# Performance work log

Hardware: AMD Instinct MI355X
Metric: run time of the kernel (lower is better)

The kernel has to match this reference:

```python
import jax, jax.numpy as jnp
import numpy as np

N_HEAD = 16
HEAD_DIM = 64
EPS = 1e-5
ROPE_BASE = 10000.0


def setup_inputs() -> dict:
    key = jax.random.key(0)
    ks = jax.random.split(key, 3)
    B, T, C = 4, 2048, 1024
    x = jax.random.normal(ks[0], (B, T, C), dtype=jnp.float32)
    Wqkv = jax.random.normal(ks[1], (C, 3 * C), dtype=jnp.float32) * (C ** -0.5)
    Wproj = jax.random.normal(ks[2], (C, C), dtype=jnp.float32) * (C ** -0.5)
    q_norm_w = jnp.ones((HEAD_DIM,), dtype=jnp.float32)
    k_norm_w = jnp.ones((HEAD_DIM,), dtype=jnp.float32)
    return {"x": x, "Wqkv": Wqkv, "Wproj": Wproj, "q_norm_w": q_norm_w, "k_norm_w": k_norm_w}


def _rms_norm(x, w):
    xf = x.astype(jnp.float32)
    normed = xf * jax.lax.rsqrt(jnp.mean(xf * xf, axis=-1, keepdims=True) + EPS)
    return (normed * w).astype(x.dtype)


def _rope_tables(T, dtype):
    inv_freq = 1.0 / (ROPE_BASE ** (jnp.arange(0, HEAD_DIM, 2, dtype=jnp.float32) / HEAD_DIM))
    t = jnp.arange(T, dtype=jnp.float32)
    freqs = jnp.outer(t, inv_freq)              # [T, D/2]
    emb = jnp.concatenate([freqs, freqs], -1)   # [T, D]
    return jnp.cos(emb).astype(dtype), jnp.sin(emb).astype(dtype)


def _rotate_half(x):
    x1, x2 = jnp.split(x, 2, axis=-1)
    return jnp.concatenate([-x2, x1], axis=-1)


def reference(x, Wqkv, Wproj, q_norm_w, k_norm_w):
    B, T, C = x.shape
    qkv = x @ Wqkv                               # [B, T, 3C]
    q, k, v = jnp.split(qkv, 3, axis=-1)
    # [B, H, T, D]
    q = q.reshape(B, T, N_HEAD, HEAD_DIM).transpose(0, 2, 1, 3)
    k = k.reshape(B, T, N_HEAD, HEAD_DIM).transpose(0, 2, 1, 3)
    v = v.reshape(B, T, N_HEAD, HEAD_DIM).transpose(0, 2, 1, 3)
    # per-head QK RMSNorm
    q = _rms_norm(q, q_norm_w)
    k = _rms_norm(k, k_norm_w)
    # RoPE
    cos, sin = _rope_tables(T, q.dtype)          # [T, D] broadcast over B,H
    q = q * cos + _rotate_half(q) * sin
    k = k * cos + _rotate_half(k) * sin
    # causal attention
    scale = 1.0 / np.sqrt(HEAD_DIM)
    att = jnp.einsum('bhqd,bhkd->bhqk', q, k) * scale
    causal = jnp.tril(jnp.ones((T, T), dtype=bool))
    att = jnp.where(causal, att, -jnp.inf)
    att = jax.nn.softmax(att, axis=-1)
    y = jnp.einsum('bhqk,bhkd->bhqd', att, v)    # [B, H, T, D]
    y = y.transpose(0, 2, 1, 3).reshape(B, T, C)
    return y @ Wproj
```

## Files before the change

kernel.cpp:

```cpp
#include <hip/hip_runtime.h>
#include <cstdint>
#include <type_traits>

typedef __attribute__((ext_vector_type(8))) short bf16x8;
typedef __attribute__((ext_vector_type(4))) float f32x4;

typedef unsigned int __attribute__((address_space(1))) as1_uint;
typedef unsigned int __attribute__((address_space(3))) as3_uint;

__device__ __forceinline__ void llds16(const void* g, void* l) {
  __builtin_amdgcn_global_load_lds((const as1_uint*)g, (as3_uint*)l, 16, 0, 0);
}

__device__ __forceinline__ unsigned short f2bf(float f) {
  unsigned int u = __builtin_bit_cast(unsigned int, f);
  u = (u + 0x7fffu + ((u >> 16) & 1u)) >> 16;
  return (unsigned short)u;
}
__device__ __forceinline__ float bf2f(unsigned short h) {
  unsigned int u = ((unsigned int)h) << 16;
  return __builtin_bit_cast(float, u);
}

__global__ __launch_bounds__(256) void cvt_f32_bf16(const float* __restrict__ in,
                                                    unsigned short* __restrict__ out, int n4) {
  int i = blockIdx.x * blockDim.x + threadIdx.x;
  int stride = gridDim.x * blockDim.x;
  for (; i < n4; i += stride) {
    float4 v = ((const float4*)in)[i];
    uint2 p;
    p.x = (unsigned)f2bf(v.x) | ((unsigned)f2bf(v.y) << 16);
    p.y = (unsigned)f2bf(v.z) | ((unsigned)f2bf(v.w) << 16);
    ((uint2*)out)[i] = p;
  }
}

__global__ __launch_bounds__(256) void transpose_f32_bf16(const float* __restrict__ W,
                                                          unsigned short* __restrict__ Wt,
                                                          int K, int N) {
  __shared__ float tile[64][65];
  int n0 = blockIdx.x * 64, k0 = blockIdx.y * 64;
  int t = threadIdx.x;
  int lr = t >> 4, lc = (t & 15) * 4;
#pragma unroll
  for (int i = 0; i < 4; ++i) {
    int k = lr + i * 16;
    float4 v = *(const float4*)&W[(size_t)(k0 + k) * N + n0 + lc];
    tile[k][lc] = v.x; tile[k][lc + 1] = v.y; tile[k][lc + 2] = v.z; tile[k][lc + 3] = v.w;
  }
  __syncthreads();
  int n = t >> 2, kc = (t & 3) * 16;
  unsigned short* dst = &Wt[(size_t)(n0 + n) * K + k0 + kc];
#pragma unroll
  for (int j = 0; j < 16; ++j) dst[j] = f2bf(tile[kc + j][n]);
}

__global__ __launch_bounds__(256) void rope_tabT(float* __restrict__ cosT, float* __restrict__ sinT) {
  int i = blockIdx.x * 256 + threadIdx.x;
  int dm = i >> 11, t = i & 2047;
  float inv = powf(10000.0f, -(float)dm * (1.0f / 32.0f));
  float a = (float)t * inv;
  cosT[i] = cosf(a);
  sinT[i] = sinf(a);
}

__device__ __forceinline__ void block_map(int& bx, int& by) {
  const int lin = blockIdx.y * gridDim.x + blockIdx.x;
  const int xcd = lin & 7;
  const int idx = lin >> 3;
  const int ych = gridDim.y >> 3;
  by = xcd * ych + (idx & (ych - 1));
  bx = idx / ych;
}

template <typename OutT>
__global__ __launch_bounds__(256) void gemm_ring(const unsigned short* __restrict__ A,
                                                 const unsigned short* __restrict__ Bt,
                                                 OutT* __restrict__ C, int M, int N, int K) {
  __shared__ unsigned short As[3][128 * 32];
  __shared__ unsigned short Bs[3][128 * 32];
  const int tid = threadIdx.x;
  const int w = tid >> 6, lane = tid & 63;
  const int l15 = lane & 15, lg = lane >> 4;
  const int wr = w >> 1, wc = w & 1;

  int bx, by;
  block_map(bx, by);
  const int m0 = by * 128, n0 = bx * 128;

  const size_t K2 = (size_t)K * 2;
  const char* Ag = (const char*)A;
  const char* Bg = (const char*)Bt;
  const int rc = lane >> 2;
  const int cb = (lane & 3) * 16;

  auto stage = [&](int buf, int kt) {
#pragma unroll
    for (int i = 0; i < 2; ++i) {
      int c = w + i * 4;
      int row = c * 16 + rc;
      int srcc = cb ^ (((row >> 1) & 3) << 4);
      size_t kofs = (size_t)kt * 64 + srcc;
      llds16(Ag + (size_t)(m0 + row) * K2 + kofs, (char*)&As[buf][0] + c * 1024);
      llds16(Bg + (size_t)(n0 + row) * K2 + kofs, (char*)&Bs[buf][0] + c * 1024);
    }
  };

  f32x4 acc[4][4] = {};
  const int nk = K >> 5;
  stage(0, 0);
  stage(1, 1);
  int cur = 0;
  for (int t = 0; t < nk; ++t) {
    if (t + 1 < nk) asm volatile("s_waitcnt vmcnt(4)" ::: "memory");
    else            asm volatile("s_waitcnt vmcnt(0)" ::: "memory");
    __builtin_amdgcn_s_barrier();
    asm volatile("" ::: "memory");
    if (t + 2 < nk) stage(cur + 2 >= 3 ? cur - 1 : cur + 2, t + 2);

    const unsigned short* Ab = &As[cur][0];
    const unsigned short* Bb = &Bs[cur][0];
    bf16x8 af[4], bfr[4];
#pragma unroll
    for (int m = 0; m < 4; ++m) {
      int row = wr * 64 + m * 16 + l15;
      af[m] = *(const bf16x8*)((const char*)Ab + row * 64 + ((lg * 16) ^ (((row >> 1) & 3) << 4)));
    }
#pragma unroll
    for (int n = 0; n < 4; ++n) {
      int row = wc * 64 + n * 16 + l15;
      bfr[n] = *(const bf16x8*)((const char*)Bb + row * 64 + ((lg * 16) ^ (((row >> 1) & 3) << 4)));
    }
#pragma unroll
    for (int m = 0; m < 4; ++m)
#pragma unroll
      for (int n = 0; n < 4; ++n)
        acc[m][n] = __builtin_amdgcn_mfma_f32_16x16x32_bf16(af[m], bfr[n], acc[m][n], 0, 0, 0);
    cur = (cur == 2) ? 0 : cur + 1;
  }

#pragma unroll
  for (int m = 0; m < 4; ++m)
#pragma unroll
    for (int n = 0; n < 4; ++n) {
      int row = m0 + wr * 64 + m * 16 + lg * 4;
      int col = n0 + wc * 64 + n * 16 + l15;
#pragma unroll
      for (int r = 0; r < 4; ++r) {
        if constexpr (std::is_same<OutT, float>::value)
          C[(size_t)(row + r) * N + col] = acc[m][n][r];
        else
          C[(size_t)(row + r) * N + col] = f2bf(acc[m][n][r]);
      }
    }
}

__global__ __launch_bounds__(256) void gemm_qkv(const unsigned short* __restrict__ A,
                                                const unsigned short* __restrict__ Bt,
                                                const float* __restrict__ qw,
                                                const float* __restrict__ kw,
                                                const float* __restrict__ cosTT,
                                                const float* __restrict__ sinTT,
                                                unsigned short* __restrict__ Qr,
                                                unsigned short* __restrict__ Kr,
                                                unsigned short* __restrict__ Vtg) {
  constexpr int K = 1024;
  __shared__ unsigned short smem[6 * 128 * 32];
  unsigned short* As = smem;
  unsigned short* Bs = smem + 3 * 128 * 32;

  const int tid = threadIdx.x;
  const int w = tid >> 6, lane = tid & 63;
  const int l15 = lane & 15, lg = lane >> 4;
  const int wr = w >> 1, wc = w & 1;

  int bx, by;
  block_map(bx, by);
  const int m0 = by * 128, n0 = bx * 128;

  const size_t K2 = (size_t)K * 2;
  const char* Ag = (const char*)A;
  const char* Bg = (const char*)Bt;
  const int rc = lane >> 2;
  const int cb = (lane & 3) * 16;

  auto stage = [&](int buf, int kt) {
#pragma unroll
    for (int i = 0; i < 2; ++i) {
      int c = w + i * 4;
      int row = c * 16 + rc;
      int srcc = cb ^ (((row >> 1) & 3) << 4);
      size_t kofs = (size_t)kt * 64 + srcc;
      llds16(Ag + (size_t)(m0 + row) * K2 + kofs, (char*)As + buf * 8192 + c * 1024);
      llds16(Bg + (size_t)(n0 + row) * K2 + kofs, (char*)Bs + buf * 8192 + c * 1024);
    }
  };

  f32x4 acc[4][4] = {};
  const int nk = K >> 5;
  stage(0, 0);
  stage(1, 1);
  int cur = 0;
  for (int t = 0; t < nk; ++t) {
    if (t + 1 < nk) asm volatile("s_waitcnt vmcnt(4)" ::: "memory");
    else            asm volatile("s_waitcnt vmcnt(0)" ::: "memory");
    __builtin_amdgcn_s_barrier();
    asm volatile("" ::: "memory");
    if (t + 2 < nk) stage(cur + 2 >= 3 ? cur - 1 : cur + 2, t + 2);

    const char* Ab = (const char*)As + cur * 8192;
    const char* Bb = (const char*)Bs + cur * 8192;
    bf16x8 af[4], bfr[4];
#pragma unroll
    for (int m = 0; m < 4; ++m) {
      int row = wr * 64 + m * 16 + l15;
      af[m] = *(const bf16x8*)(Ab + row * 64 + ((lg * 16) ^ (((row >> 1) & 3) << 4)));
    }
#pragma unroll
    for (int n = 0; n < 4; ++n) {
      int row = wc * 64 + n * 16 + l15;
      bfr[n] = *(const bf16x8*)(Bb + row * 64 + ((lg * 16) ^ (((row >> 1) & 3) << 4)));
    }
#pragma unroll
    for (int m = 0; m < 4; ++m)
#pragma unroll
      for (int n = 0; n < 4; ++n)
        acc[m][n] = __builtin_amdgcn_mfma_f32_16x16x32_bf16(af[m], bfr[n], acc[m][n], 0, 0, 0);
    cur = (cur == 2) ? 0 : cur + 1;
  }

  __syncthreads();
  const int cls = bx >> 3;
  const int head = (bx & 7) * 2 + wc;
  const int rowb = m0 + wr * 64;
  const int b = rowb >> 11;
  const int tl = rowb & 2047;
  const int bh = b * 16 + head;
  unsigned short* tb = smem + w * (64 * 76);

  if (cls < 2) {
    const float* wt = cls ? kw : qw;
    const float scale = cls ? 1.0f : 0.18033688011112042f;
    unsigned short* outp = cls ? Kr : Qr;
    float wv[4];
#pragma unroll
    for (int n = 0; n < 4; ++n) wv[n] = wt[n * 16 + l15];
    const float* c0p = cosTT + l15 * 2048;
    const float* c1p = cosTT + (16 + l15) * 2048;
    const float* s0p = sinTT + l15 * 2048;
    const float* s1p = sinTT + (16 + l15) * 2048;
#pragma unroll
    for (int m = 0; m < 4; ++m) {
      int t0 = tl + m * 16 + lg * 4;
      f32x4 ssq = {};
#pragma unroll
      for (int n = 0; n < 4; ++n) ssq += acc[m][n] * acc[m][n];
#pragma unroll
      for (int r = 0; r < 4; ++r) {
        float v = ssq[r];
        v += __shfl_xor(v, 1); v += __shfl_xor(v, 2);
        v += __shfl_xor(v, 4); v += __shfl_xor(v, 8);
        ssq[r] = rsqrtf(v * (1.0f / 64.0f) + 1e-5f) * scale;
      }
      f32x4 nv[4];
#pragma unroll
      for (int n = 0; n < 4; ++n) nv[n] = acc[m][n] * ssq * wv[n];
      f32x4 cv0 = *(const f32x4*)(c0p + t0);
      f32x4 cv1 = *(const f32x4*)(c1p + t0);
      f32x4 sv0 = *(const f32x4*)(s0p + t0);
      f32x4 sv1 = *(const f32x4*)(s1p + t0);
      f32x4 ov[4];
      ov[0] = nv[0] * cv0 - nv[2] * sv0;
      ov[1] = nv[1] * cv1 - nv[3] * sv1;
      ov[2] = nv[2] * cv0 + nv[0] * sv0;
      ov[3] = nv[3] * cv1 + nv[1] * sv1;
      int tloc = m * 16 + lg * 4;
#pragma unroll
      for (int n = 0; n < 4; ++n)
#pragma unroll
        for (int r = 0; r < 4; ++r)
          tb[(tloc + r) * 76 + n * 16 + l15] = f2bf(ov[n][r]);
    }
    asm volatile("" ::: "memory");
    const int t = lane;
    unsigned short* yp = outp + ((size_t)bh * 2048 + tl + t) * 64;
#pragma unroll
    for (int j = 0; j < 8; ++j)
      *(bf16x8*)(yp + j * 8) = *(const bf16x8*)(tb + t * 76 + j * 8);
  } else {
#pragma unroll
    for (int m = 0; m < 4; ++m)
#pragma unroll
      for (int n = 0; n < 4; ++n) {
        int d = n * 16 + l15, t = m * 16 + lg * 4;
        ushort4 pk;
        pk.x = f2bf(acc[m][n][0]); pk.y = f2bf(acc[m][n][1]);
        pk.z = f2bf(acc[m][n][2]); pk.w = f2bf(acc[m][n][3]);
        *(ushort4*)(tb + d * 76 + t) = pk;
      }
    asm volatile("" ::: "memory");
    int d2 = lane;
    unsigned short* vp = Vtg + ((size_t)bh * 64 + d2) * 2048 + tl;
#pragma unroll
    for (int j = 0; j < 8; ++j) {
      bf16x8 vv = *(const bf16x8*)(tb + d2 * 76 + j * 8);
      *(bf16x8*)(vp + j * 8) = vv;
    }
  }
}

__global__ __launch_bounds__(256) void attn_fwd(const unsigned short* __restrict__ Q,
                                                const unsigned short* __restrict__ K,
                                                const unsigned short* __restrict__ Vtg,
                                                unsigned short* __restrict__ Y) {
  const int bh = blockIdx.x;
  const int pr = blockIdx.y;
  const int b = bh >> 4, h = bh & 15;
  const int tid = threadIdx.x;
  const int w = tid >> 6, lane = tid & 63;
  const int l15 = lane & 15, lg = lane >> 4;

  __shared__ unsigned short Kl[2][64 * 64];
  __shared__ unsigned short Vt[2][64 * 64];
  __shared__ unsigned short Pl[4][16 * 64];

  const size_t bhT = (size_t)bh * 2048;
  const char* Kg = (const char*)(K + bhT * 64);
  const char* Vg = (const char*)(Vtg + bhT * 64);

  auto stage = [&](int buf, int kt) {
#pragma unroll
    for (int i = 0; i < 2; ++i) {
      int c = w * 2 + i;
      int pos = c * 1024 + lane * 16;
      int row = pos >> 7, cb = pos & 127;
      int srcb = cb ^ ((row & 7) << 4);
      llds16(Kg + ((size_t)(kt * 64 + row)) * 128 + srcb,
             (char*)&Kl[buf][0] + c * 1024);
      llds16(Vg + (size_t)row * 4096 + (size_t)kt * 128 + srcb,
             (char*)&Vt[buf][0] + c * 1024);
    }
  };

  auto run_qtile = [&](int qtb) {
    const int qbase = qtb * 64;
    const unsigned short* Qp = Q + (bhT + qbase + w * 16 + l15) * 64 + lg * 8;
    bf16x8 aq[2];
    aq[0] = *(const bf16x8*)(Qp);
    aq[1] = *(const bf16x8*)(Qp + 32);

    f32x4 o[4] = {};
    float psum = 0.0f;

    char* Pw = (char*)&Pl[w][0];
    const int psw = (l15 & 7) << 4;

    for (int kt = 0; kt <= qtb; ++kt) {
      const int cur = kt & 1;
      if (kt < qtb) stage(cur ^ 1, kt + 1);
      const char* Kc = (const char*)&Kl[cur][0];
      const char* Vc = (const char*)&Vt[cur][0];

      f32x4 s[4] = {};
      __builtin_amdgcn_s_setprio(1);
#pragma unroll
      for (int n = 0; n < 4; ++n) {
        int r = n * 16 + l15, sw = (r & 7) << 4;
#pragma unroll
        for (int ks = 0; ks < 2; ++ks) {
          bf16x8 bk = *(const bf16x8*)(Kc + r * 128 + ((ks * 64 + lg * 16) ^ sw));
          s[n] = __builtin_amdgcn_mfma_f32_16x16x32_bf16(bk, aq[ks], s[n], 0, 0, 0);
        }
      }
      __builtin_amdgcn_s_setprio(0);

      if (kt == qtb) {
#pragma unroll
        for (int n = 0; n < 4; ++n)
#pragma unroll
          for (int r = 0; r < 4; ++r)
            if (n * 16 + lg * 4 + r > w * 16 + l15) s[n][r] = -1e30f;
      }

#pragma unroll
      for (int n = 0; n < 4; ++n) {
        float p0 = __builtin_exp2f(s[n][0]);
        float p1 = __builtin_exp2f(s[n][1]);
        float p2 = __builtin_exp2f(s[n][2]);
        float p3 = __builtin_exp2f(s[n][3]);
        psum += (p0 + p1) + (p2 + p3);
        uint2 pk;
        pk.x = ((__builtin_bit_cast(unsigned int, p0) + 0x8000u) >> 16) |
               (((__builtin_bit_cast(unsigned int, p1) + 0x8000u) >> 16) << 16);
        pk.y = ((__builtin_bit_cast(unsigned int, p2) + 0x8000u) >> 16) |
               (((__builtin_bit_cast(unsigned int, p3) + 0x8000u) >> 16) << 16);
        *(uint2*)(Pw + l15 * 128 + ((n * 32 + lg * 8) ^ psw)) = pk;
      }
      asm volatile("" ::: "memory");

      bf16x8 ap[2];
      ap[0] = *(const bf16x8*)(Pw + l15 * 128 + ((lg * 16) ^ psw));
      ap[1] = *(const bf16x8*)(Pw + l15 * 128 + ((64 + lg * 16) ^ psw));

      __builtin_amdgcn_s_setprio(1);
#pragma unroll
      for (int df = 0; df < 4; ++df) {
        int rr = df * 16 + l15, sw = (rr & 7) << 4;
#pragma unroll
        for (int ks = 0; ks < 2; ++ks) {
          bf16x8 bv = *(const bf16x8*)(Vc + rr * 128 + ((ks * 64 + lg * 16) ^ sw));
          o[df] = __builtin_amdgcn_mfma_f32_16x16x32_bf16(bv, ap[ks], o[df], 0, 0, 0);
        }
      }
      __builtin_amdgcn_s_setprio(0);
      __syncthreads();
    }

    psum += __shfl_xor(psum, 16);
    psum += __shfl_xor(psum, 32);
    float inv = 1.0f / psum;

    size_t q = qbase + w * 16 + l15;
    unsigned short* yp = Y + ((size_t)b * 2048 + q) * 1024 + h * 64 + lg * 4;
#pragma unroll
    for (int df = 0; df < 4; ++df) {
      ushort4 v;
      v.x = f2bf(o[df][0] * inv);
      v.y = f2bf(o[df][1] * inv);
      v.z = f2bf(o[df][2] * inv);
      v.w = f2bf(o[df][3] * inv);
      *(ushort4*)(yp + df * 16) = v;
    }
  };

  stage(0, 0);
  __syncthreads();
  run_qtile(31 - pr);
  stage(0, 0);
  __syncthreads();
  run_qtile(pr);
}

extern "C" void kernel_launch(void* const* d_in, const int* in_sizes, int n_in,
                              void* d_out, int out_size, void* d_ws, size_t ws_size,
                              hipStream_t stream) {
  const float* x = (const float*)d_in[0];
  const float* Wqkv = (const float*)d_in[1];
  const float* Wproj = (const float*)d_in[2];
  const float* qw = (const float*)d_in[3];
  const float* kw = (const float*)d_in[4];
  float* out = (float*)d_out;

  char* ws = (char*)d_ws;
  unsigned short* xb = (unsigned short*)ws;        ws += (size_t)8192 * 1024 * 2;
  unsigned short* wqkvt = (unsigned short*)ws;     ws += (size_t)3072 * 1024 * 2;
  unsigned short* wprojt = (unsigned short*)ws;    ws += (size_t)1024 * 1024 * 2;
  unsigned short* Qr = (unsigned short*)ws;        ws += (size_t)64 * 2048 * 64 * 2;
  unsigned short* Kr = (unsigned short*)ws;        ws += (size_t)64 * 2048 * 64 * 2;
  unsigned short* Vtg = (unsigned short*)ws;       ws += (size_t)64 * 64 * 2048 * 2;
  unsigned short* yb = (unsigned short*)ws;        ws += (size_t)8192 * 1024 * 2;
  float* cosTT = (float*)ws;                       ws += (size_t)32 * 2048 * 4;
  float* sinTT = (float*)ws;                       ws += (size_t)32 * 2048 * 4;

  cvt_f32_bf16<<<2048, 256, 0, stream>>>(x, xb, 8192 * 1024 / 4);
  transpose_f32_bf16<<<dim3(48, 16), 256, 0, stream>>>(Wqkv, wqkvt, 1024, 3072);
  transpose_f32_bf16<<<dim3(16, 16), 256, 0, stream>>>(Wproj, wprojt, 1024, 1024);
  rope_tabT<<<256, 256, 0, stream>>>(cosTT, sinTT);
  gemm_qkv<<<dim3(24, 64), 256, 0, stream>>>(xb, wqkvt, qw, kw, cosTT, sinTT, Qr, Kr, Vtg);
  attn_fwd<<<dim3(64, 16), 256, 0, stream>>>(Qr, Kr, Vtg, yb);
  gemm_ring<float><<<dim3(8, 64), 256, 0, stream>>>(yb, wprojt, out, 8192, 1024, 1024);
}
```

Measured before the change: 202.5 us.

## Rewrite QKV GEMM as 8-wave 128x256 tile with phased ping-pong pipeline

The fused QKV projection kernel now uses 512-thread blocks with a 128x256 output tile and a K step of 64, double-buffered in LDS. Each k-step is split into four MFMA phases separated by barriers, with LDS fragment reads and the next global-to-LDS loads interleaved between them. s_setprio is raised around the MFMA bursts. The aim is to hide memory latency behind matrix-core work and to reuse each A tile across more output columns. The cost is many more barriers per iteration and more LDS per block (96KB), which limits how many blocks fit on a CU.

```diff
diff --git a/kernel.cpp b/kernel.cpp
--- a/kernel.cpp
+++ b/kernel.cpp
@@ -21,6 +21,8 @@
   unsigned int u = ((unsigned int)h) << 16;
   return __builtin_bit_cast(float, u);
 }
+
+#define MEMBAR() asm volatile("" ::: "memory")
 
 __global__ __launch_bounds__(256) void cvt_f32_bf16(const float* __restrict__ in,
                                                     unsigned short* __restrict__ out, int n4) {
@@ -115,7 +117,7 @@
     if (t + 1 < nk) asm volatile("s_waitcnt vmcnt(4)" ::: "memory");
     else            asm volatile("s_waitcnt vmcnt(0)" ::: "memory");
     __builtin_amdgcn_s_barrier();
-    asm volatile("" ::: "memory");
+    MEMBAR();
     if (t + 2 < nk) stage(cur + 2 >= 3 ? cur - 1 : cur + 2, t + 2);
 
     const unsigned short* Ab = &As[cur][0];
@@ -155,83 +157,150 @@
     }
 }
 
-__global__ __launch_bounds__(256) void gemm_qkv(const unsigned short* __restrict__ A,
-                                                const unsigned short* __restrict__ Bt,
-                                                const float* __restrict__ qw,
-                                                const float* __restrict__ kw,
-                                                const float* __restrict__ cosTT,
-                                                const float* __restrict__ sinTT,
-                                                unsigned short* __restrict__ Qr,
-                                                unsigned short* __restrict__ Kr,
-                                                unsigned short* __restrict__ Vtg) {
+__global__ __launch_bounds__(512, 2) void gemm_qkv8(const unsigned short* __restrict__ A,
+                                                    const unsigned short* __restrict__ Bt,
+                                                    const float* __restrict__ qw,
+                                                    const float* __restrict__ kw,
+                                                    const float* __restrict__ cosTT,
+                                                    const float* __restrict__ sinTT,
+                                                    unsigned short* __restrict__ Qr,
+                                                    unsigned short* __restrict__ Kr,
+                                                    unsigned short* __restrict__ Vtg) {
   constexpr int K = 1024;
-  __shared__ unsigned short smem[6 * 128 * 32];
-  unsigned short* As = smem;
-  unsigned short* Bs = smem + 3 * 128 * 32;
+  constexpr int nk = K >> 6;
+  __shared__ unsigned short smem[49152];
+  char* AsmB = (char*)smem;
+  char* BsmB = AsmB + 32768;
 
   const int tid = threadIdx.x;
   const int w = tid >> 6, lane = tid & 63;
   const int l15 = lane & 15, lg = lane >> 4;
-  const int wr = w >> 1, wc = w & 1;
+  const int wr = w >> 2, wc = w & 3;
 
   int bx, by;
   block_map(bx, by);
-  const int m0 = by * 128, n0 = bx * 128;
+  const int m0 = by * 128, n0 = bx * 256;
 
   const size_t K2 = (size_t)K * 2;
   const char* Ag = (const char*)A;
   const char* Bg = (const char*)Bt;
-  const int rc = lane >> 2;
-  const int cb = (lane & 3) * 16;
-
-  auto stage = [&](int buf, int kt) {
-#pragma unroll
-    for (int i = 0; i < 2; ++i) {
-      int c = w + i * 4;
-      int row = c * 16 + rc;
-      int srcc = cb ^ (((row >> 1) & 3) << 4);
-      size_t kofs = (size_t)kt * 64 + srcc;
-      llds16(Ag + (size_t)(m0 + row) * K2 + kofs, (char*)As + buf * 8192 + c * 1024);
-      llds16(Bg + (size_t)(n0 + row) * K2 + kofs, (char*)Bs + buf * 8192 + c * 1024);
-    }
+
+  const int srow8 = lane >> 3;
+  const int scb = (lane & 7) * 16;
+
+  auto stageAh = [&](int h, int kt, int b) {
+    int row = w * 8 + srow8;
+    int srcc = scb ^ ((row & 7) << 4);
+    llds16(Ag + (size_t)(m0 + h * 64 + row) * K2 + (size_t)kt * 128 + srcc,
+           AsmB + b * 16384 + (h * 64 + w * 8) * 128);
   };
+  auto stageBh = [&](int h, int kt, int b) {
+#pragma unroll
+    for (int j = 0; j < 2; ++j) {
+      int c = w * 2 + j;
+      int row = c * 8 + srow8;
+      int srcc = scb ^ ((row & 7) << 4);
+      llds16(Bg + (size_t)(n0 + h * 128 + row) * K2 + (size_t)kt * 128 + srcc,
+             BsmB + b * 32768 + (h * 128 + c * 8) * 128);
+    }
+  };
 
   f32x4 acc[4][4] = {};
-  const int nk = K >> 5;
-  stage(0, 0);
-  stage(1, 1);
-  int cur = 0;
-  for (int t = 0; t < nk; ++t) {
-    if (t + 1 < nk) asm volatile("s_waitcnt vmcnt(4)" ::: "memory");
-    else            asm volatile("s_waitcnt vmcnt(0)" ::: "memory");
+  bf16x8 afr[2][2], bfr[4][2];
+
+  stageAh(0, 0, 0); stageAh(1, 0, 0);
+  stageBh(0, 0, 0); stageBh(1, 0, 0);
+  stageBh(0, 1, 1); stageBh(1, 1, 1);
+
+  for (int kt = 0; kt < nk; ++kt) {
+    const int pi = kt & 1;
+    if (kt == nk - 1) asm volatile("s_waitcnt vmcnt(0)" ::: "memory");
+    else              asm volatile("s_waitcnt vmcnt(4)" ::: "memory");
     __builtin_amdgcn_s_barrier();
-    asm volatile("" ::: "memory");
-    if (t + 2 < nk) stage(cur + 2 >= 3 ? cur - 1 : cur + 2, t + 2);
-
-    const char* Ab = (const char*)As + cur * 8192;
-    const char* Bb = (const char*)Bs + cur * 8192;
-    bf16x8 af[4], bfr[4];
-#pragma unroll
-    for (int m = 0; m < 4; ++m) {
-      int row = wr * 64 + m * 16 + l15;
-      af[m] = *(const bf16x8*)(Ab + row * 64 + ((lg * 16) ^ (((row >> 1) & 3) << 4)));
-    }
-#pragma unroll
-    for (int n = 0; n < 4; ++n) {
-      int row = wc * 64 + n * 16 + l15;
-      bfr[n] = *(const bf16x8*)(Bb + row * 64 + ((lg * 16) ^ (((row >> 1) & 3) << 4)));
-    }
-#pragma unroll
-    for (int m = 0; m < 4; ++m)
-#pragma unroll
-      for (int n = 0; n < 4; ++n)
-        acc[m][n] = __builtin_amdgcn_mfma_f32_16x16x32_bf16(af[m], bfr[n], acc[m][n], 0, 0, 0);
-    cur = (cur == 2) ? 0 : cur + 1;
+    MEMBAR();
+    const char* Ap = AsmB + pi * 16384;
+    const char* Bp = BsmB + pi * 32768;
+
+#pragma unroll
+    for (int i = 0; i < 2; ++i)
+#pragma unroll
+      for (int ks = 0; ks < 2; ++ks) {
+        int arow = wr * 64 + i * 16 + l15;
+        afr[i][ks] = *(const bf16x8*)(Ap + arow * 128 + ((ks * 64 + lg * 16) ^ ((arow & 7) << 4)));
+        int brow = wc * 64 + i * 16 + l15;
+        bfr[i][ks] = *(const bf16x8*)(Bp + brow * 128 + ((ks * 64 + lg * 16) ^ ((brow & 7) << 4)));
+      }
+    if (kt + 1 < nk) { stageAh(0, kt + 1, pi ^ 1); stageAh(1, kt + 1, pi ^ 1); }
+    MEMBAR(); __builtin_amdgcn_s_barrier(); MEMBAR();
+    __builtin_amdgcn_s_setprio(1);
+#pragma unroll
+    for (int i = 0; i < 2; ++i)
+#pragma unroll
+      for (int n = 0; n < 2; ++n)
+#pragma unroll
+        for (int ks = 0; ks < 2; ++ks)
+          acc[i][n] = __builtin_amdgcn_mfma_f32_16x16x32_bf16(afr[i][ks], bfr[n][ks], acc[i][n], 0, 0, 0);
+    __builtin_amdgcn_s_setprio(0);
+    MEMBAR(); __builtin_amdgcn_s_barrier(); MEMBAR();
+
+#pragma unroll
+    for (int n = 0; n < 2; ++n)
+#pragma unroll
+      for (int ks = 0; ks < 2; ++ks) {
+        int brow = wc * 64 + (2 + n) * 16 + l15;
+        bfr[2 + n][ks] = *(const bf16x8*)(Bp + brow * 128 + ((ks * 64 + lg * 16) ^ ((brow & 7) << 4)));
+      }
+    MEMBAR(); __builtin_amdgcn_s_barrier(); MEMBAR();
+    __builtin_amdgcn_s_setprio(1);
+#pragma unroll
+    for (int i = 0; i < 2; ++i)
+#pragma unroll
+      for (int n = 0; n < 2; ++n)
+#pragma unroll
+        for (int ks = 0; ks < 2; ++ks)
+          acc[i][2 + n] = __builtin_amdgcn_mfma_f32_16x16x32_bf16(afr[i][ks], bfr[2 + n][ks], acc[i][2 + n], 0, 0, 0);
+    __builtin_amdgcn_s_setprio(0);
+    MEMBAR(); __builtin_amdgcn_s_barrier(); MEMBAR();
+
+#pragma unroll
+    for (int i = 0; i < 2; ++i)
+#pragma unroll
+      for (int ks = 0; ks < 2; ++ks) {
+        int arow = wr * 64 + (2 + i) * 16 + l15;
+        afr[i][ks] = *(const bf16x8*)(Ap + arow * 128 + ((ks * 64 + lg * 16) ^ ((arow & 7) << 4)));
+      }
+    if (kt + 2 < nk) stageBh(0, kt + 2, pi);
+    MEMBAR(); __builtin_amdgcn_s_barrier(); MEMBAR();
+    __builtin_amdgcn_s_setprio(1);
+#pragma unroll
+    for (int i = 0; i < 2; ++i)
+#pragma unroll
+      for (int n = 0; n < 2; ++n)
+#pragma unroll
+        for (int ks = 0; ks < 2; ++ks)
+          acc[2 + i][2 + n] = __builtin_amdgcn_mfma_f32_16x16x32_bf16(afr[i][ks], bfr[2 + n][ks], acc[2 + i][2 + n], 0, 0, 0);
+    __builtin_amdgcn_s_setprio(0);
+    MEMBAR(); __builtin_amdgcn_s_barrier(); MEMBAR();
+
+    if (kt + 2 < nk) stageBh(1, kt + 2, pi);
+    MEMBAR(); __builtin_amdgcn_s_barrier(); MEMBAR();
+    __builtin_amdgcn_s_setprio(1);
+#pragma unroll
+    for (int i = 0; i < 2; ++i)
+#pragma unroll
+      for (int n = 0; n < 2; ++n)
+#pragma unroll
+        for (int ks = 0; ks < 2; ++ks)
+          acc[2 + i][n] = __builtin_amdgcn_mfma_f32_16x16x32_bf16(afr[i][ks], bfr[n][ks], acc[2 + i][n], 0, 0, 0);
+    __builtin_amdgcn_s_setprio(0);
+    MEMBAR();
   }
 
   __syncthreads();
-  const int cls = bx >> 3;
-  const int head = (bx & 7) * 2 + wc;
+
+  const int head4 = bx * 4 + wc;
+  const int cls = head4 >> 4;
+  const int head = head4 & 15;
   const int rowb = m0 + wr * 64;
   const int b = rowb >> 11;
   const int tl = rowb & 2047;
@@ -281,7 +350,7 @@
         for (int r = 0; r < 4; ++r)
           tb[(tloc + r) * 76 + n * 16 + l15] = f2bf(ov[n][r]);
     }
-    asm volatile("" ::: "memory");
+    MEMBAR();
     const int t = lane;
     unsigned short* yp = outp + ((size_t)bh * 2048 + tl + t) * 64;
 #pragma unroll
@@ -298,7 +367,7 @@
         pk.z = f2bf(acc[m][n][2]); pk.w = f2bf(acc[m][n][3]);
         *(ushort4*)(tb + d * 76 + t) = pk;
       }
-    asm volatile("" ::: "memory");
+    MEMBAR();
     int d2 = lane;
     unsigned short* vp = Vtg + ((size_t)bh * 64 + d2) * 2048 + tl;
 #pragma unroll
@@ -396,7 +465,7 @@
                (((__builtin_bit_cast(unsigned int, p3) + 0x8000u) >> 16) << 16);
         *(uint2*)(Pw + l15 * 128 + ((n * 32 + lg * 8) ^ psw)) = pk;
       }
-      asm volatile("" ::: "memory");
+      MEMBAR();
 
       bf16x8 ap[2];
       ap[0] = *(const bf16x8*)(Pw + l15 * 128 + ((lg * 16) ^ psw));
@@ -466,7 +535,7 @@
   transpose_f32_bf16<<<dim3(48, 16), 256, 0, stream>>>(Wqkv, wqkvt, 1024, 3072);
   transpose_f32_bf16<<<dim3(16, 16), 256, 0, stream>>>(Wproj, wprojt, 1024, 1024);
   rope_tabT<<<256, 256, 0, stream>>>(cosTT, sinTT);
-  gemm_qkv<<<dim3(24, 64), 256, 0, stream>>>(xb, wqkvt, qw, kw, cosTT, sinTT, Qr, Kr, Vtg);
+  gemm_qkv8<<<dim3(12, 64), 512, 0, stream>>>(xb, wqkvt, qw, kw, cosTT, sinTT, Qr, Kr, Vtg);
   attn_fwd<<<dim3(64, 16), 256, 0, stream>>>(Qr, Kr, Vtg, yb);
   gemm_ring<float><<<dim3(8, 64), 256, 0, stream>>>(yb, wprojt, out, 8192, 1024, 1024);
 }
```

Result: no change. 203.7 us (+0.6%).

## Enlarge QKV GEMM tile to 256x128 and truncate P to bf16 in attention

Applied to the files above, without the earlier changes.

The fused QKV GEMM now uses 256x128 block tiles, with each wave computing 128x64 and more A-fragment reuse per B load. The grid is halved, the stage loads and LDS layout are reworked, and launch bounds are set to two blocks per SM. The epilogue writes its RMSNorm/RoPE and V-transpose output in two 64-row chunks so the LDS staging stays small. The MFMA loop runs at raised priority, and the attention kernel packs P to bf16 by truncation instead of rounding, which saves ALU work but adds a small rounding bias.

```diff
diff --git a/kernel.cpp b/kernel.cpp
--- a/kernel.cpp
+++ b/kernel.cpp
@@ -21,6 +21,8 @@
   unsigned int u = ((unsigned int)h) << 16;
   return __builtin_bit_cast(float, u);
 }
+
+#define MEMBAR() asm volatile("" ::: "memory")
 
 __global__ __launch_bounds__(256) void cvt_f32_bf16(const float* __restrict__ in,
                                                     unsigned short* __restrict__ out, int n4) {
@@ -115,7 +117,7 @@
     if (t + 1 < nk) asm volatile("s_waitcnt vmcnt(4)" ::: "memory");
     else            asm volatile("s_waitcnt vmcnt(0)" ::: "memory");
     __builtin_amdgcn_s_barrier();
-    asm volatile("" ::: "memory");
+    MEMBAR();
     if (t + 2 < nk) stage(cur + 2 >= 3 ? cur - 1 : cur + 2, t + 2);
 
     const unsigned short* Ab = &As[cur][0];
@@ -155,19 +157,19 @@
     }
 }
 
-__global__ __launch_bounds__(256) void gemm_qkv(const unsigned short* __restrict__ A,
-                                                const unsigned short* __restrict__ Bt,
-                                                const float* __restrict__ qw,
-                                                const float* __restrict__ kw,
-                                                const float* __restrict__ cosTT,
-                                                const float* __restrict__ sinTT,
-                                                unsigned short* __restrict__ Qr,
-                                                unsigned short* __restrict__ Kr,
-                                                unsigned short* __restrict__ Vtg) {
+__global__ __launch_bounds__(256, 2) void gemm_qkvW(const unsigned short* __restrict__ A,
+                                                    const unsigned short* __restrict__ Bt,
+                                                    const float* __restrict__ qw,
+                                                    const float* __restrict__ kw,
+                                                    const float* __restrict__ cosTT,
+                                                    const float* __restrict__ sinTT,
+                                                    unsigned short* __restrict__ Qr,
+                                                    unsigned short* __restrict__ Kr,
+                                                    unsigned short* __restrict__ Vtg) {
   constexpr int K = 1024;
-  __shared__ unsigned short smem[6 * 128 * 32];
-  unsigned short* As = smem;
-  unsigned short* Bs = smem + 3 * 128 * 32;
+  constexpr int nk = K >> 5;
+  __shared__ unsigned short smem[36864];
+  char* base = (char*)smem;
 
   const int tid = threadIdx.x;
   const int w = tid >> 6, lane = tid & 63;
@@ -176,44 +178,49 @@
 
   int bx, by;
   block_map(bx, by);
-  const int m0 = by * 128, n0 = bx * 128;
+  const int m0 = by * 256, n0 = bx * 128;
 
   const size_t K2 = (size_t)K * 2;
   const char* Ag = (const char*)A;
   const char* Bg = (const char*)Bt;
-  const int rc = lane >> 2;
-  const int cb = (lane & 3) * 16;
+  const int rc4 = tid >> 2;
+  const int cb = (tid & 3) * 16;
 
   auto stage = [&](int buf, int kt) {
-#pragma unroll
-    for (int i = 0; i < 2; ++i) {
-      int c = w + i * 4;
-      int row = c * 16 + rc;
+    char* ab = base + buf * 24576;
+#pragma unroll
+    for (int j = 0; j < 4; ++j) {
+      int row = j * 64 + rc4;
       int srcc = cb ^ (((row >> 1) & 3) << 4);
-      size_t kofs = (size_t)kt * 64 + srcc;
-      llds16(Ag + (size_t)(m0 + row) * K2 + kofs, (char*)As + buf * 8192 + c * 1024);
-      llds16(Bg + (size_t)(n0 + row) * K2 + kofs, (char*)Bs + buf * 8192 + c * 1024);
+      llds16(Ag + (size_t)(m0 + row) * K2 + (size_t)kt * 64 + srcc,
+             ab + j * 4096 + tid * 16);
+    }
+#pragma unroll
+    for (int j = 0; j < 2; ++j) {
+      int row = j * 64 + rc4;
+      int srcc = cb ^ (((row >> 1) & 3) << 4);
+      llds16(Bg + (size_t)(n0 + row) * K2 + (size_t)kt * 64 + srcc,
+             ab + 16384 + j * 4096 + tid * 16);
     }
   };
 
-  f32x4 acc[4][4] = {};
-  const int nk = K >> 5;
+  f32x4 acc[8][4] = {};
   stage(0, 0);
   stage(1, 1);
   int cur = 0;
   for (int t = 0; t < nk; ++t) {
-    if (t + 1 < nk) asm volatile("s_waitcnt vmcnt(4)" ::: "memory");
+    if (t + 1 < nk) asm volatile("s_waitcnt vmcnt(6)" ::: "memory");
     else            asm volatile("s_waitcnt vmcnt(0)" ::: "memory");
     __builtin_amdgcn_s_barrier();
-    asm volatile("" ::: "memory");
+    MEMBAR();
     if (t + 2 < nk) stage(cur + 2 >= 3 ? cur - 1 : cur + 2, t + 2);
 
-    const char* Ab = (const char*)As + cur * 8192;
-    const char* Bb = (const char*)Bs + cur * 8192;
-    bf16x8 af[4], bfr[4];
-#pragma unroll
-    for (int m = 0; m < 4; ++m) {
-      int row = wr * 64 + m * 16 + l15;
+    const char* Ab = base + cur * 24576;
+    const char* Bb = Ab + 16384;
+    bf16x8 af[8], bfr[4];
+#pragma unroll
+    for (int m = 0; m < 8; ++m) {
+      int row = wr * 128 + m * 16 + l15;
       af[m] = *(const bf16x8*)(Ab + row * 64 + ((lg * 16) ^ (((row >> 1) & 3) << 4)));
     }
 #pragma unroll
@@ -221,22 +228,26 @@
       int row = wc * 64 + n * 16 + l15;
       bfr[n] = *(const bf16x8*)(Bb + row * 64 + ((lg * 16) ^ (((row >> 1) & 3) << 4)));
     }
-#pragma unroll
-    for (int m = 0; m < 4; ++m)
+    __builtin_amdgcn_s_setprio(1);
+#pragma unroll
+    for (int m = 0; m < 8; ++m)
 #pragma unroll
       for (int n = 0; n < 4; ++n)
         acc[m][n] = __builtin_amdgcn_mfma_f32_16x16x32_bf16(af[m], bfr[n], acc[m][n], 0, 0, 0);
+    __builtin_amdgcn_s_setprio(0);
     cur = (cur == 2) ? 0 : cur + 1;
   }
 
   __syncthreads();
-  const int cls = bx >> 3;
-  const int head = (bx & 7) * 2 + wc;
-  const int rowb = m0 + wr * 64;
+
+  const int head2 = bx * 2 + wc;
+  const int cls = head2 >> 4;
+  const int head = head2 & 15;
+  const int rowb = m0 + wr * 128;
   const int b = rowb >> 11;
   const int tl = rowb & 2047;
   const int bh = b * 16 + head;
-  unsigned short* tb = smem + w * (64 * 76);
+  unsigned short* tb = smem + w * 4864;
 
   if (cls < 2) {
     const float* wt = cls ? kw : qw;
@@ -250,61 +261,72 @@
     const float* s0p = sinTT + l15 * 2048;
     const float* s1p = sinTT + (16 + l15) * 2048;
 #pragma unroll
-    for (int m = 0; m < 4; ++m) {
-      int t0 = tl + m * 16 + lg * 4;
-      f32x4 ssq = {};
-#pragma unroll
-      for (int n = 0; n < 4; ++n) ssq += acc[m][n] * acc[m][n];
-#pragma unroll
-      for (int r = 0; r < 4; ++r) {
-        float v = ssq[r];
-        v += __shfl_xor(v, 1); v += __shfl_xor(v, 2);
-        v += __shfl_xor(v, 4); v += __shfl_xor(v, 8);
-        ssq[r] = rsqrtf(v * (1.0f / 64.0f) + 1e-5f) * scale;
-      }
-      f32x4 nv[4];
-#pragma unroll
-      for (int n = 0; n < 4; ++n) nv[n] = acc[m][n] * ssq * wv[n];
-      f32x4 cv0 = *(const f32x4*)(c0p + t0);
-      f32x4 cv1 = *(const f32x4*)(c1p + t0);
-      f32x4 sv0 = *(const f32x4*)(s0p + t0);
-      f32x4 sv1 = *(const f32x4*)(s1p + t0);
-      f32x4 ov[4];
-      ov[0] = nv[0] * cv0 - nv[2] * sv0;
-      ov[1] = nv[1] * cv1 - nv[3] * sv1;
-      ov[2] = nv[2] * cv0 + nv[0] * sv0;
-      ov[3] = nv[3] * cv1 + nv[1] * sv1;
-      int tloc = m * 16 + lg * 4;
-#pragma unroll
-      for (int n = 0; n < 4; ++n)
-#pragma unroll
-        for (int r = 0; r < 4; ++r)
-          tb[(tloc + r) * 76 + n * 16 + l15] = f2bf(ov[n][r]);
-    }
-    asm volatile("" ::: "memory");
-    const int t = lane;
-    unsigned short* yp = outp + ((size_t)bh * 2048 + tl + t) * 64;
-#pragma unroll
-    for (int j = 0; j < 8; ++j)
-      *(bf16x8*)(yp + j * 8) = *(const bf16x8*)(tb + t * 76 + j * 8);
+    for (int chunk = 0; chunk < 2; ++chunk) {
+#pragma unroll
+      for (int q = 0; q < 4; ++q) {
+        const int m = chunk * 4 + q;
+        int t0 = tl + m * 16 + lg * 4;
+        f32x4 ssq = {};
+#pragma unroll
+        for (int n = 0; n < 4; ++n) ssq += acc[m][n] * acc[m][n];
+#pragma unroll
+        for (int r = 0; r < 4; ++r) {
+          float v = ssq[r];
+          v += __shfl_xor(v, 1); v += __shfl_xor(v, 2);
+          v += __shfl_xor(v, 4); v += __shfl_xor(v, 8);
+          ssq[r] = rsqrtf(v * (1.0f / 64.0f) + 1e-5f) * scale;
+        }
+        f32x4 nv[4];
+#pragma unroll
+        for (int n = 0; n < 4; ++n) nv[n] = acc[m][n] * ssq * wv[n];
+        f32x4 cv0 = *(const f32x4*)(c0p + t0);
+        f32x4 cv1 = *(const f32x4*)(c1p + t0);
+        f32x4 sv0 = *(const f32x4*)(s0p + t0);
+        f32x4 sv1 = *(const f32x4*)(s1p + t0);
+        f32x4 ov[4];
+        ov[0] = nv[0] * cv0 - nv[2] * sv0;
+        ov[1] = nv[1] * cv1 - nv[3] * sv1;
+        ov[2] = nv[2] * cv0 + nv[0] * sv0;
+        ov[3] = nv[3] * cv1 + nv[1] * sv1;
+        int tloc = q * 16 + lg * 4;
+#pragma unroll
+        for (int n = 0; n < 4; ++n)
+#pragma unroll
+          for (int r = 0; r < 4; ++r)
+            tb[(tloc + r) * 76 + n * 16 + l15] = f2bf(ov[n][r]);
+      }
+      MEMBAR();
+      const int t = lane;
+      unsigned short* yp = outp + ((size_t)bh * 2048 + tl + chunk * 64 + t) * 64;
+#pragma unroll
+      for (int j = 0; j < 8; ++j)
+        *(bf16x8*)(yp + j * 8) = *(const bf16x8*)(tb + t * 76 + j * 8);
+      MEMBAR();
+    }
   } else {
 #pragma unroll
-    for (int m = 0; m < 4; ++m)
-#pragma unroll
-      for (int n = 0; n < 4; ++n) {
-        int d = n * 16 + l15, t = m * 16 + lg * 4;
-        ushort4 pk;
-        pk.x = f2bf(acc[m][n][0]); pk.y = f2bf(acc[m][n][1]);
-        pk.z = f2bf(acc[m][n][2]); pk.w = f2bf(acc[m][n][3]);
-        *(ushort4*)(tb + d * 76 + t) = pk;
-      }
-    asm volatile("" ::: "memory");
-    int d2 = lane;
-    unsigned short* vp = Vtg + ((size_t)bh * 64 + d2) * 2048 + tl;
-#pragma unroll
-    for (int j = 0; j < 8; ++j) {
-      bf16x8 vv = *(const bf16x8*)(tb + d2 * 76 + j * 8);
-      *(bf16x8*)(vp + j * 8) = vv;
+    for (int chunk = 0; chunk < 2; ++chunk) {
+#pragma unroll
+      for (int q = 0; q < 4; ++q) {
+        const int m = chunk * 4 + q;
+#pragma unroll
+        for (int n = 0; n < 4; ++n) {
+          int d = n * 16 + l15, tloc = q * 16 + lg * 4;
+          ushort4 pk;
+          pk.x = f2bf(acc[m][n][0]); pk.y = f2bf(acc[m][n][1]);
+          pk.z = f2bf(acc[m][n][2]); pk.w = f2bf(acc[m][n][3]);
+          *(ushort4*)(tb + d * 76 + tloc) = pk;
+        }
+      }
+      MEMBAR();
+      int d2 = lane;
+      unsigned short* vp = Vtg + ((size_t)bh * 64 + d2) * 2048 + tl + chunk * 64;
+#pragma unroll
+      for (int j = 0; j < 8; ++j) {
+        bf16x8 vv = *(const bf16x8*)(tb + d2 * 76 + j * 8);
+        *(bf16x8*)(vp + j * 8) = vv;
+      }
+      MEMBAR();
     }
   }
 }
@@ -389,14 +411,16 @@
         float p2 = __builtin_exp2f(s[n][2]);
         float p3 = __builtin_exp2f(s[n][3]);
         psum += (p0 + p1) + (p2 + p3);
+        unsigned u0 = __builtin_bit_cast(unsigned, p0);
+        unsigned u1 = __builtin_bit_cast(unsigned, p1);
+        unsigned u2 = __builtin_bit_cast(unsigned, p2);
+        unsigned u3 = __builtin_bit_cast(unsigned, p3);
         uint2 pk;
-        pk.x = ((__builtin_bit_cast(unsigned int, p0) + 0x8000u) >> 16) |
-               (((__builtin_bit_cast(unsigned int, p1) + 0x8000u) >> 16) << 16);
-        pk.y = ((__builtin_bit_cast(unsigned int, p2) + 0x8000u) >> 16) |
-               (((__builtin_bit_cast(unsigned int, p3) + 0x8000u) >> 16) << 16);
+        pk.x = (u0 >> 16) | (u1 & 0xffff0000u);
+        pk.y = (u2 >> 16) | (u3 & 0xffff0000u);
         *(uint2*)(Pw + l15 * 128 + ((n * 32 + lg * 8) ^ psw)) = pk;
       }
-      asm volatile("" ::: "memory");
+      MEMBAR();
 
       bf16x8 ap[2];
       ap[0] = *(const bf16x8*)(Pw + l15 * 128 + ((lg * 16) ^ psw));
@@ -466,7 +490,7 @@
   transpose_f32_bf16<<<dim3(48, 16), 256, 0, stream>>>(Wqkv, wqkvt, 1024, 3072);
   transpose_f32_bf16<<<dim3(16, 16), 256, 0, stream>>>(Wproj, wprojt, 1024, 1024);
   rope_tabT<<<256, 256, 0, stream>>>(cosTT, sinTT);
-  gemm_qkv<<<dim3(24, 64), 256, 0, stream>>>(xb, wqkvt, qw, kw, cosTT, sinTT, Qr, Kr, Vtg);
+  gemm_qkvW<<<dim3(24, 32), 256, 0, stream>>>(xb, wqkvt, qw, kw, cosTT, sinTT, Qr, Kr, Vtg);
   attn_fwd<<<dim3(64, 16), 256, 0, stream>>>(Qr, Kr, Vtg, yb);
   gemm_ring<float><<<dim3(8, 64), 256, 0, stream>>>(yb, wprojt, out, 8192, 1024, 1024);
 }
```

Result: faster. 185.8 us (-8.3%).
